# Optimization experiments

Hardware: AMD Instinct MI355X
Metric: run time of the kernel (lower is better)

## Reference

```python
import jax, jax.numpy as jnp
import numpy as np

N = 262144          # nodes
E = N * 16          # edges (avg degree 16)
C_IN = 64
C_OUT = 64
GRID = 0.5          # voxel size
POS_EXTENT = 10.0   # pos in [0, 10)^3
NVOX_DIM = int(round(POS_EXTENT / GRID))  # 20
NVOX = NVOX_DIM ** 3                      # 8000 voxels
BN_EPS = 1e-5


def setup_inputs() -> dict:
    key = jax.random.key(0)
    k = jax.random.split(key, 5)
    x = jax.random.normal(k[0], (N, C_IN), dtype=jnp.float32)
    pos = jax.random.uniform(k[1], (N, 3), dtype=jnp.float32, minval=0.0, maxval=POS_EXTENT)
    edge_index = jax.random.randint(k[2], (2, E), 0, N, dtype=jnp.int32)
    W = jax.random.normal(k[3], (C_IN, C_OUT), dtype=jnp.float32) / np.float32(np.sqrt(C_IN))
    b = jnp.zeros((C_OUT,), jnp.float32)
    gamma = jnp.ones((C_OUT,), jnp.float32)
    beta = jnp.zeros((C_OUT,), jnp.float32)
    return {"x": x, "pos": pos, "edge_index": edge_index,
            "W": W, "b": b, "gamma": gamma, "beta": beta}


def reference(x, pos, edge_index, W, b, gamma, beta):
    # --- self.down: Linear -> BatchNorm1d (training-mode batch stats) -> ReLU ---
    h = x @ W + b                                   # [N, C_OUT]
    mean = jnp.mean(h, axis=0)
    var = jnp.mean(jnp.square(h - mean), axis=0)    # biased variance (torch BN)
    h = (h - mean) * jax.lax.rsqrt(var + BN_EPS) * gamma + beta
    h = jax.nn.relu(h)

    # --- max_pool_neighbor_x: scatter-max of neighbor features (self-loops added) ---
    row, col = edge_index[0], edge_index[1]
    pooled = jax.ops.segment_max(h[row], col, num_segments=N)  # [N, C_OUT]
    h = jnp.maximum(pooled, h)  # self-loop; also fixes -inf for isolated nodes

    # --- GridSampling: voxel-grid quantize + per-voxel mean of x and pos ---
    vid = jnp.clip(jnp.floor(pos / GRID).astype(jnp.int32), 0, NVOX_DIM - 1)  # [N,3]
    vox = (vid[:, 0] * NVOX_DIM + vid[:, 1]) * NVOX_DIM + vid[:, 2]           # [N]
    cnt = jax.ops.segment_sum(jnp.ones((N,), jnp.float32), vox, num_segments=NVOX)
    x_sum = jax.ops.segment_sum(h, vox, num_segments=NVOX)     # [NVOX, C_OUT]
    p_sum = jax.ops.segment_sum(pos, vox, num_segments=NVOX)   # [NVOX, 3]
    denom = jnp.maximum(cnt, 1.0)[:, None]
    x_out = x_sum / denom
    pos_out = p_sum / denom
    # concat features and positions of the downsampled graph: [NVOX, C_OUT+3]
    return jnp.concatenate([x_out, pos_out], axis=1)
```

## Files before the change

### kernel.cpp

```cpp
#include <hip/hip_runtime.h>
#include <hip/hip_fp16.h>

#define NVOX_DIM 20
#define NVOX 8000
#define BN_EPS 1e-5f

#define NBUCK 1024
#define BSHIFT 8
#define NODES_PER_BUCK 256
#define GEMM_BLOCKS 1024
#define ZERO_BLOCKS 64
#define CAP 5120

typedef _Float16 f16x8 __attribute__((ext_vector_type(8)));
typedef float f32x4 __attribute__((ext_vector_type(4)));

__device__ __forceinline__ unsigned short f2key(float v) {
    unsigned short hb = __half_as_ushort(__float2half(v));
    unsigned short m = (unsigned short)(0x8000u | (unsigned short)(-(int)(hb >> 15)));
    return (unsigned short)(hb ^ m);
}

__global__ __launch_bounds__(256) void k0_fused(const float* __restrict__ x,
                                                const float* __restrict__ W,
                                                const float* __restrict__ bias,
                                                unsigned short* __restrict__ h16,
                                                float* __restrict__ partials, int n16,
                                                float4* __restrict__ zero_zone,
                                                int zero_n4) {
    __shared__ float sW[4096];
    __shared__ float red[2][4][64];
    int t = threadIdx.x;

    if (blockIdx.x >= GEMM_BLOCKS) {
        int zb = blockIdx.x - GEMM_BLOCKS;
        float4 z = {0.f, 0.f, 0.f, 0.f};
        for (int i = zb * 256 + t; i < zero_n4; i += ZERO_BLOCKS * 256) zero_zone[i] = z;
        return;
    }

    for (int i = t; i < 4096; i += 256) sW[i] = W[i];
    __syncthreads();
    int lane = t & 63;
    int w = t >> 6;
    int l15 = lane & 15;
    int q = lane >> 4;

    f16x8 bf[4][2];
#pragma unroll
    for (int t4 = 0; t4 < 4; ++t4)
#pragma unroll
        for (int kb = 0; kb < 2; ++kb)
#pragma unroll
            for (int i = 0; i < 8; ++i)
                bf[t4][kb][i] = (_Float16)sW[(kb * 32 + q * 8 + i) * 64 + t4 * 16 + l15];
    float bv[4];
#pragma unroll
    for (int t4 = 0; t4 < 4; ++t4) bv[t4] = bias[t4 * 16 + l15];

    float s[4] = {0.f, 0.f, 0.f, 0.f}, s2[4] = {0.f, 0.f, 0.f, 0.f};

    for (int g = blockIdx.x * 4 + w; g < n16; g += GEMM_BLOCKS * 4) {
        int row0 = g * 16;
        const float* xp = x + (size_t)(row0 + l15) * 64 + q * 8;
        float4 xa = *(const float4*)(xp);
        float4 xb = *(const float4*)(xp + 4);
        float4 xc = *(const float4*)(xp + 32);
        float4 xd = *(const float4*)(xp + 36);
        f16x8 a0, a1;
        a0[0] = (_Float16)xa.x; a0[1] = (_Float16)xa.y; a0[2] = (_Float16)xa.z; a0[3] = (_Float16)xa.w;
        a0[4] = (_Float16)xb.x; a0[5] = (_Float16)xb.y; a0[6] = (_Float16)xb.z; a0[7] = (_Float16)xb.w;
        a1[0] = (_Float16)xc.x; a1[1] = (_Float16)xc.y; a1[2] = (_Float16)xc.z; a1[3] = (_Float16)xc.w;
        a1[4] = (_Float16)xd.x; a1[5] = (_Float16)xd.y; a1[6] = (_Float16)xd.z; a1[7] = (_Float16)xd.w;

#pragma unroll
        for (int t4 = 0; t4 < 4; ++t4) {
            f32x4 acc = {bv[t4], bv[t4], bv[t4], bv[t4]};
            acc = __builtin_amdgcn_mfma_f32_16x16x32_f16(a0, bf[t4][0], acc, 0, 0, 0);
            acc = __builtin_amdgcn_mfma_f32_16x16x32_f16(a1, bf[t4][1], acc, 0, 0, 0);
            s[t4] += acc[0] + acc[1] + acc[2] + acc[3];
            s2[t4] = fmaf(acc[0], acc[0], s2[t4]);
            s2[t4] = fmaf(acc[1], acc[1], s2[t4]);
            s2[t4] = fmaf(acc[2], acc[2], s2[t4]);
            s2[t4] = fmaf(acc[3], acc[3], s2[t4]);
#pragma unroll
            for (int r = 0; r < 4; ++r) {
                h16[(size_t)(row0 + q * 4 + r) * 64 + t4 * 16 + l15] = f2key(acc[r]);
            }
        }
    }

#pragma unroll
    for (int t4 = 0; t4 < 4; ++t4) {
        s[t4] += __shfl_xor(s[t4], 16, 64);
        s[t4] += __shfl_xor(s[t4], 32, 64);
        s2[t4] += __shfl_xor(s2[t4], 16, 64);
        s2[t4] += __shfl_xor(s2[t4], 32, 64);
    }
    if (lane < 16) {
#pragma unroll
        for (int t4 = 0; t4 < 4; ++t4) {
            red[0][w][t4 * 16 + lane] = s[t4];
            red[1][w][t4 * 16 + lane] = s2[t4];
        }
    }
    __syncthreads();
    if (t < 128) {
        int c = t & 63;
        int which = t >> 6;
        float v = red[which][0][c] + red[which][1][c] + red[which][2][c] + red[which][3][c];
        partials[(size_t)blockIdx.x * 128 + which * 64 + c] = v;
    }
}

__global__ __launch_bounds__(1024) void k3_finalize(const float* __restrict__ partials,
                                                    const float* __restrict__ gamma,
                                                    const float* __restrict__ beta,
                                                    float* __restrict__ stats2, float invN) {
    __shared__ float red[8][128];
    __shared__ float tot[128];
    int t = threadIdx.x;
    int c = t & 127;
    int g = t >> 7;
    float s = 0.f;
    for (int b = g; b < GEMM_BLOCKS; b += 8) s += partials[(size_t)b * 128 + c];
    red[g][c] = s;
    __syncthreads();
    if (t < 128) {
        float v = 0.f;
#pragma unroll
        for (int g2 = 0; g2 < 8; ++g2) v += red[g2][t];
        tot[t] = v;
    }
    __syncthreads();
    if (t < 64) {
        float mean = tot[t] * invN;
        float var = tot[64 + t] * invN - mean * mean;
        float sc = gamma[t] * rsqrtf(var + BN_EPS);
        stats2[t] = sc;
        stats2[64 + t] = beta[t] - mean * sc;
    }
}

__global__ __launch_bounds__(1024) void k_bin(const int* __restrict__ rows,
                                              const int* __restrict__ cols,
                                              int* __restrict__ cursor,
                                              unsigned int* __restrict__ pairs, int E) {
    __shared__ int lh[NBUCK];
    __shared__ int lpos[NBUCK];
    int t = threadIdx.x;
    lh[t] = 0;
    __syncthreads();
    int base = blockIdx.x * 16384 + t * 16;
    int r[16], c[16];
#pragma unroll
    for (int g4 = 0; g4 < 4; ++g4) {
        int e = base + g4 * 4;
        int4 r4 = *(const int4*)(rows + e);
        int4 c4 = *(const int4*)(cols + e);
        r[g4 * 4 + 0] = r4.x; c[g4 * 4 + 0] = c4.x;
        r[g4 * 4 + 1] = r4.y; c[g4 * 4 + 1] = c4.y;
        r[g4 * 4 + 2] = r4.z; c[g4 * 4 + 2] = c4.z;
        r[g4 * 4 + 3] = r4.w; c[g4 * 4 + 3] = c4.w;
    }
#pragma unroll
    for (int i = 0; i < 16; ++i) atomicAdd(&lh[c[i] >> BSHIFT], 1);
    __syncthreads();
    int res = atomicAdd(&cursor[t], lh[t]);
    lpos[t] = res;
    __syncthreads();
#pragma unroll
    for (int i = 0; i < 16; ++i) {
        int bkt = c[i] >> BSHIFT;
        int idx = atomicAdd(&lpos[bkt], 1);
        if (idx < CAP)
            pairs[(size_t)bkt * CAP + idx] =
                ((unsigned int)r[i] << 8) | (unsigned int)(c[i] & (NODES_PER_BUCK - 1));
    }
}

__global__ __launch_bounds__(1024) void k_pool(const unsigned int* __restrict__ pairs,
                                               const int* __restrict__ cursor,
                                               const unsigned short* __restrict__ h16,
                                               const float* __restrict__ pos,
                                               const float* __restrict__ stats2,
                                               float* __restrict__ xs,
                                               float* __restrict__ ps,
                                               float* __restrict__ cnt) {
    __shared__ unsigned int tile[NODES_PER_BUCK * 64];
    int b = blockIdx.x;
    int t = threadIdx.x;
    int lane = t & 63;
    int w = t >> 6;
    float scale = stats2[lane];
    float shift = stats2[64 + lane];

    const unsigned int* src = (const unsigned int*)(h16 + (size_t)b * (NODES_PER_BUCK * 64));
#pragma unroll
    for (int k = 0; k < 8; ++k) {
        int i = t + k * 1024;
        unsigned int u = src[i];
        tile[2 * i] = u & 0xFFFFu;
        tile[2 * i + 1] = u >> 16;
    }
    __syncthreads();

    int cntE = min(cursor[b], CAP);
    int start = b * CAP;
    int end = start + cntE;
    int chunk = (cntE + 15) >> 4;
    int cs = start + w * chunk;
    int ce = min(cs + chunk, end);
    for (int j0 = cs; j0 < ce; j0 += 64) {
        int lim = min(64, ce - j0);
        unsigned int pk = (lane < lim) ? pairs[j0 + lane] : 0u;
        int jj = 0;
        for (; jj + 16 <= lim; jj += 16) {
            unsigned int qv[16], vv[16];
#pragma unroll
            for (int u = 0; u < 16; ++u) qv[u] = __shfl(pk, jj + u, 64);
#pragma unroll
            for (int u = 0; u < 16; ++u) vv[u] = h16[(size_t)(qv[u] >> 8) * 64 + lane];
#pragma unroll
            for (int u = 0; u < 16; ++u)
                atomicMax(&tile[((qv[u] & 255u) << 6) + lane], vv[u]);
        }
        for (; jj < lim; ++jj) {
            unsigned int qq = __shfl(pk, jj, 64);
            unsigned int v = h16[(size_t)(qq >> 8) * 64 + lane];
            atomicMax(&tile[((qq & 255u) << 6) + lane], v);
        }
    }
    __syncthreads();

#pragma unroll
    for (int nl = 0; nl < NODES_PER_BUCK; nl += 16) {
        int node_l = nl + w;
        int c = (b << BSHIFT) + node_l;
        float px = pos[(size_t)c * 3 + 0];
        float py = pos[(size_t)c * 3 + 1];
        float pz = pos[(size_t)c * 3 + 2];
        int v0 = min(max((int)floorf(px * 2.f), 0), NVOX_DIM - 1);
        int v1 = min(max((int)floorf(py * 2.f), 0), NVOX_DIM - 1);
        int v2 = min(max((int)floorf(pz * 2.f), 0), NVOX_DIM - 1);
        int vox = (v0 * NVOX_DIM + v1) * NVOX_DIM + v2;
        unsigned int k = tile[(node_l << 6) + lane];
        unsigned short hb = (k & 0x8000u) ? (unsigned short)(k ^ 0x8000u)
                                          : (unsigned short)(0xFFFFu ^ k);
        __half_raw hr;
        hr.x = hb;
        float v = __half2float((__half)hr);
        float val = fmaxf(fmaf(v, scale, shift), 0.f);
        atomicAdd(&xs[(size_t)vox * 64 + lane], val);
        if (lane < 3) atomicAdd(&ps[vox * 3 + lane], lane == 0 ? px : (lane == 1 ? py : pz));
        if (lane == 0) atomicAdd(&cnt[vox], 1.f);
    }
}

__global__ __launch_bounds__(256) void k7_out(const float* __restrict__ xs,
                                              const float* __restrict__ ps,
                                              const float* __restrict__ cnt,
                                              float* __restrict__ out, int total) {
    int idx = blockIdx.x * blockDim.x + threadIdx.x;
    if (idx >= total) return;
    int v = idx / 67;
    int c = idx - v * 67;
    float d = fmaxf(cnt[v], 1.f);
    float val = (c < 64) ? xs[(size_t)v * 64 + c] : ps[v * 3 + (c - 64)];
    out[idx] = val / d;
}

extern "C" void kernel_launch(void* const* d_in, const int* in_sizes, int n_in,
                              void* d_out, int out_size, void* d_ws, size_t ws_size,
                              hipStream_t stream) {
    const float* x     = (const float*)d_in[0];
    const float* pos   = (const float*)d_in[1];
    const int*   ei    = (const int*)d_in[2];
    const float* W     = (const float*)d_in[3];
    const float* b     = (const float*)d_in[4];
    const float* gamma = (const float*)d_in[5];
    const float* beta  = (const float*)d_in[6];
    float* out = (float*)d_out;

    const int n = in_sizes[0] / 64;
    const int E = in_sizes[2] / 2;

    char* ws = (char*)d_ws;
    unsigned short* h16      = (unsigned short*)(ws + 0);
    unsigned int*   pairs    = (unsigned int*)(ws + 33554432);
    float*          partials = (float*)(ws + 54525952);
    float*          stats2   = (float*)(ws + 55050240);
    int*            cursor   = (int*)(ws + 55051264);
    float*          xs       = (float*)(ws + 55055360);
    float*          ps       = (float*)(ws + 57103360);
    float*          cnt      = (float*)(ws + 57199360);
    float4*         zero4    = (float4*)(ws + 55051264);
    const int zero_n4 = (57231360 - 55051264) / 16;

    k0_fused<<<GEMM_BLOCKS + ZERO_BLOCKS, 256, 0, stream>>>(x, W, b, h16, partials,
                                                            n >> 4, zero4, zero_n4);
    k3_finalize<<<1, 1024, 0, stream>>>(partials, gamma, beta, stats2, 1.0f / (float)n);
    k_bin<<<E / 16384, 1024, 0, stream>>>(ei, ei + E, cursor, pairs, E);
    k_pool<<<NBUCK, 1024, 0, stream>>>(pairs, cursor, h16, pos, stats2, xs, ps, cnt);
    k7_out<<<(out_size + 255) / 256, 256, 0, stream>>>(xs, ps, cnt, out, out_size);
}
```

Before: 341.9 us.

## Fuse edge binning into GEMM kernel and vectorize pooling pair loads

Moves the edge bucketing pass into the first kernel as 256 extra 256-thread blocks, so binning runs concurrently with the GEMM blocks and one launch disappears. The cursor array is now cleared by a separate memset instead of the zero blocks. In the pool kernel, the h16 tile load uses uint4, and the pair list is read as uniform uint4 loads instead of per-lane loads plus shuffles. The per-wave chunk is rounded up to a multiple of 8 for alignment. The binning blocks re-read cols twice, and the added memset is an extra operation on the stream.

```diff
diff --git a/kernel.cpp b/kernel.cpp
--- a/kernel.cpp
+++ b/kernel.cpp
@@ -8,8 +8,9 @@
 #define NBUCK 1024
 #define BSHIFT 8
 #define NODES_PER_BUCK 256
+#define BIN_BLOCKS 256
 #define GEMM_BLOCKS 1024
-#define ZERO_BLOCKS 64
+#define ZERO_BLOCKS 16
 #define CAP 5120
 
 typedef _Float16 f16x8 __attribute__((ext_vector_type(8)));
@@ -26,19 +27,70 @@
                                                 const float* __restrict__ bias,
                                                 unsigned short* __restrict__ h16,
                                                 float* __restrict__ partials, int n16,
+                                                const int* __restrict__ rows,
+                                                const int* __restrict__ cols,
+                                                int* __restrict__ cursor,
+                                                unsigned int* __restrict__ pairs,
                                                 float4* __restrict__ zero_zone,
                                                 int zero_n4) {
     __shared__ float sW[4096];
     __shared__ float red[2][4][64];
+    __shared__ int lh[NBUCK];
+    __shared__ int lpos[NBUCK];
     int t = threadIdx.x;
 
-    if (blockIdx.x >= GEMM_BLOCKS) {
-        int zb = blockIdx.x - GEMM_BLOCKS;
+    if (blockIdx.x < BIN_BLOCKS) {
+        int bid = blockIdx.x;
+#pragma unroll
+        for (int i = t; i < NBUCK; i += 256) lh[i] = 0;
+        __syncthreads();
+#pragma unroll
+        for (int p = 0; p < 4; ++p) {
+            int base = bid * 16384 + p * 4096 + t * 16;
+#pragma unroll
+            for (int g4 = 0; g4 < 4; ++g4) {
+                int4 c4 = *(const int4*)(cols + base + g4 * 4);
+                atomicAdd(&lh[c4.x >> BSHIFT], 1);
+                atomicAdd(&lh[c4.y >> BSHIFT], 1);
+                atomicAdd(&lh[c4.z >> BSHIFT], 1);
+                atomicAdd(&lh[c4.w >> BSHIFT], 1);
+            }
+        }
+        __syncthreads();
+#pragma unroll
+        for (int i = t; i < NBUCK; i += 256)
+            lpos[i] = atomicAdd(&cursor[i], lh[i]);
+        __syncthreads();
+#pragma unroll
+        for (int p = 0; p < 4; ++p) {
+            int base = bid * 16384 + p * 4096 + t * 16;
+#pragma unroll
+            for (int g4 = 0; g4 < 4; ++g4) {
+                int4 r4 = *(const int4*)(rows + base + g4 * 4);
+                int4 c4 = *(const int4*)(cols + base + g4 * 4);
+                int rr[4] = {r4.x, r4.y, r4.z, r4.w};
+                int cc[4] = {c4.x, c4.y, c4.z, c4.w};
+#pragma unroll
+                for (int u = 0; u < 4; ++u) {
+                    int bkt = cc[u] >> BSHIFT;
+                    int idx = atomicAdd(&lpos[bkt], 1);
+                    if (idx < CAP)
+                        pairs[(size_t)bkt * CAP + idx] =
+                            ((unsigned int)rr[u] << 8) |
+                            (unsigned int)(cc[u] & (NODES_PER_BUCK - 1));
+                }
+            }
+        }
+        return;
+    }
+    if (blockIdx.x >= BIN_BLOCKS + GEMM_BLOCKS) {
+        int zb = blockIdx.x - BIN_BLOCKS - GEMM_BLOCKS;
         float4 z = {0.f, 0.f, 0.f, 0.f};
         for (int i = zb * 256 + t; i < zero_n4; i += ZERO_BLOCKS * 256) zero_zone[i] = z;
         return;
     }
 
+    int gb = blockIdx.x - BIN_BLOCKS;
     for (int i = t; i < 4096; i += 256) sW[i] = W[i];
     __syncthreads();
     int lane = t & 63;
@@ -60,7 +112,7 @@
 
     float s[4] = {0.f, 0.f, 0.f, 0.f}, s2[4] = {0.f, 0.f, 0.f, 0.f};
 
-    for (int g = blockIdx.x * 4 + w; g < n16; g += GEMM_BLOCKS * 4) {
+    for (int g = gb * 4 + w; g < n16; g += GEMM_BLOCKS * 4) {
         int row0 = g * 16;
         const float* xp = x + (size_t)(row0 + l15) * 64 + q * 8;
         float4 xa = *(const float4*)(xp);
@@ -109,7 +161,7 @@
         int c = t & 63;
         int which = t >> 6;
         float v = red[which][0][c] + red[which][1][c] + red[which][2][c] + red[which][3][c];
-        partials[(size_t)blockIdx.x * 128 + which * 64 + c] = v;
+        partials[(size_t)gb * 128 + which * 64 + c] = v;
     }
 }
 
@@ -139,43 +191,6 @@
         float sc = gamma[t] * rsqrtf(var + BN_EPS);
         stats2[t] = sc;
         stats2[64 + t] = beta[t] - mean * sc;
-    }
-}
-
-__global__ __launch_bounds__(1024) void k_bin(const int* __restrict__ rows,
-                                              const int* __restrict__ cols,
-                                              int* __restrict__ cursor,
-                                              unsigned int* __restrict__ pairs, int E) {
-    __shared__ int lh[NBUCK];
-    __shared__ int lpos[NBUCK];
-    int t = threadIdx.x;
-    lh[t] = 0;
-    __syncthreads();
-    int base = blockIdx.x * 16384 + t * 16;
-    int r[16], c[16];
-#pragma unroll
-    for (int g4 = 0; g4 < 4; ++g4) {
-        int e = base + g4 * 4;
-        int4 r4 = *(const int4*)(rows + e);
-        int4 c4 = *(const int4*)(cols + e);
-        r[g4 * 4 + 0] = r4.x; c[g4 * 4 + 0] = c4.x;
-        r[g4 * 4 + 1] = r4.y; c[g4 * 4 + 1] = c4.y;
-        r[g4 * 4 + 2] = r4.z; c[g4 * 4 + 2] = c4.z;
-        r[g4 * 4 + 3] = r4.w; c[g4 * 4 + 3] = c4.w;
-    }
-#pragma unroll
-    for (int i = 0; i < 16; ++i) atomicAdd(&lh[c[i] >> BSHIFT], 1);
-    __syncthreads();
-    int res = atomicAdd(&cursor[t], lh[t]);
-    lpos[t] = res;
-    __syncthreads();
-#pragma unroll
-    for (int i = 0; i < 16; ++i) {
-        int bkt = c[i] >> BSHIFT;
-        int idx = atomicAdd(&lpos[bkt], 1);
-        if (idx < CAP)
-            pairs[(size_t)bkt * CAP + idx] =
-                ((unsigned int)r[i] << 8) | (unsigned int)(c[i] & (NODES_PER_BUCK - 1));
     }
 }
 
@@ -195,41 +210,68 @@
     float scale = stats2[lane];
     float shift = stats2[64 + lane];
 
-    const unsigned int* src = (const unsigned int*)(h16 + (size_t)b * (NODES_PER_BUCK * 64));
-#pragma unroll
-    for (int k = 0; k < 8; ++k) {
+    const uint4* src4 = (const uint4*)(h16 + (size_t)b * (NODES_PER_BUCK * 64));
+#pragma unroll
+    for (int k = 0; k < 2; ++k) {
         int i = t + k * 1024;
-        unsigned int u = src[i];
-        tile[2 * i] = u & 0xFFFFu;
-        tile[2 * i + 1] = u >> 16;
-    }
-    __syncthreads();
-
-    int cntE = min(cursor[b], CAP);
+        uint4 u = src4[i];
+        unsigned int* d = &tile[i * 8];
+        d[0] = u.x & 0xFFFFu; d[1] = u.x >> 16;
+        d[2] = u.y & 0xFFFFu; d[3] = u.y >> 16;
+        d[4] = u.z & 0xFFFFu; d[5] = u.z >> 16;
+        d[6] = u.w & 0xFFFFu; d[7] = u.w >> 16;
+    }
+    __syncthreads();
+
+    int cntE = min(__builtin_amdgcn_readfirstlane(cursor[b]), CAP);
+    int chunk = (((cntE + 15) >> 4) + 7) & ~7;
+    int wu = __builtin_amdgcn_readfirstlane(w);
     int start = b * CAP;
-    int end = start + cntE;
-    int chunk = (cntE + 15) >> 4;
-    int cs = start + w * chunk;
-    int ce = min(cs + chunk, end);
-    for (int j0 = cs; j0 < ce; j0 += 64) {
-        int lim = min(64, ce - j0);
-        unsigned int pk = (lane < lim) ? pairs[j0 + lane] : 0u;
-        int jj = 0;
-        for (; jj + 16 <= lim; jj += 16) {
-            unsigned int qv[16], vv[16];
-#pragma unroll
-            for (int u = 0; u < 16; ++u) qv[u] = __shfl(pk, jj + u, 64);
-#pragma unroll
-            for (int u = 0; u < 16; ++u) vv[u] = h16[(size_t)(qv[u] >> 8) * 64 + lane];
-#pragma unroll
-            for (int u = 0; u < 16; ++u)
-                atomicMax(&tile[((qv[u] & 255u) << 6) + lane], vv[u]);
-        }
-        for (; jj < lim; ++jj) {
-            unsigned int qq = __shfl(pk, jj, 64);
-            unsigned int v = h16[(size_t)(qq >> 8) * 64 + lane];
-            atomicMax(&tile[((qq & 255u) << 6) + lane], v);
-        }
+    int cs = start + wu * chunk;
+    int ce = min(cs + chunk, start + cntE);
+    int j = cs;
+    for (; j + 16 <= ce; j += 16) {
+        uint4 qa = *(const uint4*)(pairs + j);
+        uint4 qb = *(const uint4*)(pairs + j + 4);
+        uint4 qc = *(const uint4*)(pairs + j + 8);
+        uint4 qd = *(const uint4*)(pairs + j + 12);
+        unsigned int v0 = h16[(size_t)(qa.x >> 8) * 64 + lane];
+        unsigned int v1 = h16[(size_t)(qa.y >> 8) * 64 + lane];
+        unsigned int v2 = h16[(size_t)(qa.z >> 8) * 64 + lane];
+        unsigned int v3 = h16[(size_t)(qa.w >> 8) * 64 + lane];
+        unsigned int v4 = h16[(size_t)(qb.x >> 8) * 64 + lane];
+        unsigned int v5 = h16[(size_t)(qb.y >> 8) * 64 + lane];
+        unsigned int v6 = h16[(size_t)(qb.z >> 8) * 64 + lane];
+        unsigned int v7 = h16[(size_t)(qb.w >> 8) * 64 + lane];
+        unsigned int v8 = h16[(size_t)(qc.x >> 8) * 64 + lane];
+        unsigned int v9 = h16[(size_t)(qc.y >> 8) * 64 + lane];
+        unsigned int va = h16[(size_t)(qc.z >> 8) * 64 + lane];
+        unsigned int vb = h16[(size_t)(qc.w >> 8) * 64 + lane];
+        unsigned int vc = h16[(size_t)(qd.x >> 8) * 64 + lane];
+        unsigned int vd = h16[(size_t)(qd.y >> 8) * 64 + lane];
+        unsigned int ve = h16[(size_t)(qd.z >> 8) * 64 + lane];
+        unsigned int vf = h16[(size_t)(qd.w >> 8) * 64 + lane];
+        atomicMax(&tile[((qa.x & 255u) << 6) + lane], v0);
+        atomicMax(&tile[((qa.y & 255u) << 6) + lane], v1);
+        atomicMax(&tile[((qa.z & 255u) << 6) + lane], v2);
+        atomicMax(&tile[((qa.w & 255u) << 6) + lane], v3);
+        atomicMax(&tile[((qb.x & 255u) << 6) + lane], v4);
+        atomicMax(&tile[((qb.y & 255u) << 6) + lane], v5);
+        atomicMax(&tile[((qb.z & 255u) << 6) + lane], v6);
+        atomicMax(&tile[((qb.w & 255u) << 6) + lane], v7);
+        atomicMax(&tile[((qc.x & 255u) << 6) + lane], v8);
+        atomicMax(&tile[((qc.y & 255u) << 6) + lane], v9);
+        atomicMax(&tile[((qc.z & 255u) << 6) + lane], va);
+        atomicMax(&tile[((qc.w & 255u) << 6) + lane], vb);
+        atomicMax(&tile[((qd.x & 255u) << 6) + lane], vc);
+        atomicMax(&tile[((qd.y & 255u) << 6) + lane], vd);
+        atomicMax(&tile[((qd.z & 255u) << 6) + lane], ve);
+        atomicMax(&tile[((qd.w & 255u) << 6) + lane], vf);
+    }
+    for (; j < ce; ++j) {
+        unsigned int qq = __builtin_amdgcn_readfirstlane(pairs[j]);
+        unsigned int v = h16[(size_t)(qq >> 8) * 64 + lane];
+        atomicMax(&tile[((qq & 255u) << 6) + lane], v);
     }
     __syncthreads();
 
@@ -294,13 +336,14 @@
     float*          xs       = (float*)(ws + 55055360);
     float*          ps       = (float*)(ws + 57103360);
     float*          cnt      = (float*)(ws + 57199360);
-    float4*         zero4    = (float4*)(ws + 55051264);
-    const int zero_n4 = (57231360 - 55051264) / 16;
-
-    k0_fused<<<GEMM_BLOCKS + ZERO_BLOCKS, 256, 0, stream>>>(x, W, b, h16, partials,
-                                                            n >> 4, zero4, zero_n4);
+    float4*         zero4    = (float4*)(ws + 55055360);
+    const int zero_n4 = (57231360 - 55055360) / 16;
+
+    hipMemsetAsync(cursor, 0, 4096, stream);
+
+    k0_fused<<<BIN_BLOCKS + GEMM_BLOCKS + ZERO_BLOCKS, 256, 0, stream>>>(
+        x, W, b, h16, partials, n >> 4, ei, ei + E, cursor, pairs, zero4, zero_n4);
     k3_finalize<<<1, 1024, 0, stream>>>(partials, gamma, beta, stats2, 1.0f / (float)n);
-    k_bin<<<E / 16384, 1024, 0, stream>>>(ei, ei + E, cursor, pairs, E);
     k_pool<<<NBUCK, 1024, 0, stream>>>(pairs, cursor, h16, pos, stats2, xs, ps, cnt);
     k7_out<<<(out_size + 255) / 256, 256, 0, stream>>>(xs, ps, cnt, out, out_size);
 }
```

After: 360.5 us. 5.4% more time.

## Halve pool bucket size, use wave-uniform vector pair loads, reorder launches

Applied to the files above, without the earlier changes.

Doubles the number of edge buckets to 2048 with 128 nodes each, so k_pool runs 512-thread blocks with a 32 KB LDS tile and more blocks can reside per CU. The per-wave pair list is now read with wave-uniform uint4 loads (scalar-friendly via readfirstlane) instead of a per-lane load followed by shuffles. The cursor array is now cleared with a separate memset, and k_bin is launched before k3_finalize. The risk is the smaller CAP of 2560 per bucket, which leaves less headroom for skewed degree distributions, plus an extra memset launch.

```diff
diff --git a/kernel.cpp b/kernel.cpp
--- a/kernel.cpp
+++ b/kernel.cpp
@@ -5,12 +5,12 @@
 #define NVOX 8000
 #define BN_EPS 1e-5f
 
-#define NBUCK 1024
-#define BSHIFT 8
-#define NODES_PER_BUCK 256
+#define NBUCK 2048
+#define BSHIFT 7
+#define NODES_PER_BUCK 128
 #define GEMM_BLOCKS 1024
-#define ZERO_BLOCKS 64
-#define CAP 5120
+#define ZERO_BLOCKS 16
+#define CAP 2560
 
 typedef _Float16 f16x8 __attribute__((ext_vector_type(8)));
 typedef float f32x4 __attribute__((ext_vector_type(4)));
@@ -150,6 +150,7 @@
     __shared__ int lpos[NBUCK];
     int t = threadIdx.x;
     lh[t] = 0;
+    lh[t + 1024] = 0;
     __syncthreads();
     int base = blockIdx.x * 16384 + t * 16;
     int r[16], c[16];
@@ -166,8 +167,8 @@
 #pragma unroll
     for (int i = 0; i < 16; ++i) atomicAdd(&lh[c[i] >> BSHIFT], 1);
     __syncthreads();
-    int res = atomicAdd(&cursor[t], lh[t]);
-    lpos[t] = res;
+    lpos[t] = atomicAdd(&cursor[t], lh[t]);
+    lpos[t + 1024] = atomicAdd(&cursor[t + 1024], lh[t + 1024]);
     __syncthreads();
 #pragma unroll
     for (int i = 0; i < 16; ++i) {
@@ -175,18 +176,19 @@
         int idx = atomicAdd(&lpos[bkt], 1);
         if (idx < CAP)
             pairs[(size_t)bkt * CAP + idx] =
-                ((unsigned int)r[i] << 8) | (unsigned int)(c[i] & (NODES_PER_BUCK - 1));
-    }
-}
-
-__global__ __launch_bounds__(1024) void k_pool(const unsigned int* __restrict__ pairs,
-                                               const int* __restrict__ cursor,
-                                               const unsigned short* __restrict__ h16,
-                                               const float* __restrict__ pos,
-                                               const float* __restrict__ stats2,
-                                               float* __restrict__ xs,
-                                               float* __restrict__ ps,
-                                               float* __restrict__ cnt) {
+                ((unsigned int)r[i] << BSHIFT) |
+                (unsigned int)(c[i] & (NODES_PER_BUCK - 1));
+    }
+}
+
+__global__ __launch_bounds__(512) void k_pool(const unsigned int* __restrict__ pairs,
+                                              const int* __restrict__ cursor,
+                                              const unsigned short* __restrict__ h16,
+                                              const float* __restrict__ pos,
+                                              const float* __restrict__ stats2,
+                                              float* __restrict__ xs,
+                                              float* __restrict__ ps,
+                                              float* __restrict__ cnt) {
     __shared__ unsigned int tile[NODES_PER_BUCK * 64];
     int b = blockIdx.x;
     int t = threadIdx.x;
@@ -198,43 +200,68 @@
     const unsigned int* src = (const unsigned int*)(h16 + (size_t)b * (NODES_PER_BUCK * 64));
 #pragma unroll
     for (int k = 0; k < 8; ++k) {
-        int i = t + k * 1024;
+        int i = t + k * 512;
         unsigned int u = src[i];
         tile[2 * i] = u & 0xFFFFu;
         tile[2 * i + 1] = u >> 16;
     }
     __syncthreads();
 
-    int cntE = min(cursor[b], CAP);
+    int cntE = min(__builtin_amdgcn_readfirstlane(cursor[b]), CAP);
+    int chunk = (((cntE + 7) >> 3) + 7) & ~7;
+    int wu = __builtin_amdgcn_readfirstlane(w);
     int start = b * CAP;
-    int end = start + cntE;
-    int chunk = (cntE + 15) >> 4;
-    int cs = start + w * chunk;
-    int ce = min(cs + chunk, end);
-    for (int j0 = cs; j0 < ce; j0 += 64) {
-        int lim = min(64, ce - j0);
-        unsigned int pk = (lane < lim) ? pairs[j0 + lane] : 0u;
-        int jj = 0;
-        for (; jj + 16 <= lim; jj += 16) {
-            unsigned int qv[16], vv[16];
-#pragma unroll
-            for (int u = 0; u < 16; ++u) qv[u] = __shfl(pk, jj + u, 64);
-#pragma unroll
-            for (int u = 0; u < 16; ++u) vv[u] = h16[(size_t)(qv[u] >> 8) * 64 + lane];
-#pragma unroll
-            for (int u = 0; u < 16; ++u)
-                atomicMax(&tile[((qv[u] & 255u) << 6) + lane], vv[u]);
-        }
-        for (; jj < lim; ++jj) {
-            unsigned int qq = __shfl(pk, jj, 64);
-            unsigned int v = h16[(size_t)(qq >> 8) * 64 + lane];
-            atomicMax(&tile[((qq & 255u) << 6) + lane], v);
-        }
-    }
-    __syncthreads();
-
-#pragma unroll
-    for (int nl = 0; nl < NODES_PER_BUCK; nl += 16) {
+    int cs = start + wu * chunk;
+    int ce = min(cs + chunk, start + cntE);
+    int j = cs;
+    for (; j + 16 <= ce; j += 16) {
+        uint4 qa = *(const uint4*)(pairs + j);
+        uint4 qb = *(const uint4*)(pairs + j + 4);
+        uint4 qc = *(const uint4*)(pairs + j + 8);
+        uint4 qd = *(const uint4*)(pairs + j + 12);
+        unsigned int v0 = h16[(size_t)(qa.x >> BSHIFT) * 64 + lane];
+        unsigned int v1 = h16[(size_t)(qa.y >> BSHIFT) * 64 + lane];
+        unsigned int v2 = h16[(size_t)(qa.z >> BSHIFT) * 64 + lane];
+        unsigned int v3 = h16[(size_t)(qa.w >> BSHIFT) * 64 + lane];
+        unsigned int v4 = h16[(size_t)(qb.x >> BSHIFT) * 64 + lane];
+        unsigned int v5 = h16[(size_t)(qb.y >> BSHIFT) * 64 + lane];
+        unsigned int v6 = h16[(size_t)(qb.z >> BSHIFT) * 64 + lane];
+        unsigned int v7 = h16[(size_t)(qb.w >> BSHIFT) * 64 + lane];
+        unsigned int v8 = h16[(size_t)(qc.x >> BSHIFT) * 64 + lane];
+        unsigned int v9 = h16[(size_t)(qc.y >> BSHIFT) * 64 + lane];
+        unsigned int va = h16[(size_t)(qc.z >> BSHIFT) * 64 + lane];
+        unsigned int vb = h16[(size_t)(qc.w >> BSHIFT) * 64 + lane];
+        unsigned int vc = h16[(size_t)(qd.x >> BSHIFT) * 64 + lane];
+        unsigned int vd = h16[(size_t)(qd.y >> BSHIFT) * 64 + lane];
+        unsigned int ve = h16[(size_t)(qd.z >> BSHIFT) * 64 + lane];
+        unsigned int vf = h16[(size_t)(qd.w >> BSHIFT) * 64 + lane];
+        const unsigned int M = NODES_PER_BUCK - 1;
+        atomicMax(&tile[((qa.x & M) << 6) + lane], v0);
+        atomicMax(&tile[((qa.y & M) << 6) + lane], v1);
+        atomicMax(&tile[((qa.z & M) << 6) + lane], v2);
+        atomicMax(&tile[((qa.w & M) << 6) + lane], v3);
+        atomicMax(&tile[((qb.x & M) << 6) + lane], v4);
+        atomicMax(&tile[((qb.y & M) << 6) + lane], v5);
+        atomicMax(&tile[((qb.z & M) << 6) + lane], v6);
+        atomicMax(&tile[((qb.w & M) << 6) + lane], v7);
+        atomicMax(&tile[((qc.x & M) << 6) + lane], v8);
+        atomicMax(&tile[((qc.y & M) << 6) + lane], v9);
+        atomicMax(&tile[((qc.z & M) << 6) + lane], va);
+        atomicMax(&tile[((qc.w & M) << 6) + lane], vb);
+        atomicMax(&tile[((qd.x & M) << 6) + lane], vc);
+        atomicMax(&tile[((qd.y & M) << 6) + lane], vd);
+        atomicMax(&tile[((qd.z & M) << 6) + lane], ve);
+        atomicMax(&tile[((qd.w & M) << 6) + lane], vf);
+    }
+    for (; j < ce; ++j) {
+        unsigned int qq = __builtin_amdgcn_readfirstlane(pairs[j]);
+        unsigned int v = h16[(size_t)(qq >> BSHIFT) * 64 + lane];
+        atomicMax(&tile[((qq & (NODES_PER_BUCK - 1)) << 6) + lane], v);
+    }
+    __syncthreads();
+
+#pragma unroll
+    for (int nl = 0; nl < NODES_PER_BUCK; nl += 8) {
         int node_l = nl + w;
         int c = (b << BSHIFT) + node_l;
         float px = pos[(size_t)c * 3 + 0];
@@ -291,16 +318,18 @@
     float*          partials = (float*)(ws + 54525952);
     float*          stats2   = (float*)(ws + 55050240);
     int*            cursor   = (int*)(ws + 55051264);
-    float*          xs       = (float*)(ws + 55055360);
-    float*          ps       = (float*)(ws + 57103360);
-    float*          cnt      = (float*)(ws + 57199360);
-    float4*         zero4    = (float4*)(ws + 55051264);
-    const int zero_n4 = (57231360 - 55051264) / 16;
+    float*          xs       = (float*)(ws + 55059456);
+    float*          ps       = (float*)(ws + 57107456);
+    float*          cnt      = (float*)(ws + 57203456);
+    float4*         zero4    = (float4*)(ws + 55059456);
+    const int zero_n4 = (57235456 - 55059456) / 16;
+
+    hipMemsetAsync(cursor, 0, NBUCK * 4, stream);
 
     k0_fused<<<GEMM_BLOCKS + ZERO_BLOCKS, 256, 0, stream>>>(x, W, b, h16, partials,
                                                             n >> 4, zero4, zero_n4);
+    k_bin<<<E / 16384, 1024, 0, stream>>>(ei, ei + E, cursor, pairs, E);
     k3_finalize<<<1, 1024, 0, stream>>>(partials, gamma, beta, stats2, 1.0f / (float)n);
-    k_bin<<<E / 16384, 1024, 0, stream>>>(ei, ei + E, cursor, pairs, E);
-    k_pool<<<NBUCK, 1024, 0, stream>>>(pairs, cursor, h16, pos, stats2, xs, ps, cnt);
+    k_pool<<<NBUCK, 512, 0, stream>>>(pairs, cursor, h16, pos, stats2, xs, ps, cnt);
     k7_out<<<(out_size + 255) / 256, 256, 0, stream>>>(xs, ps, cnt, out, out_size);
 }
```

Result: slower. 357.6 us (+4.6%).
